# Optimization experiments

Hardware: AMD Instinct MI355X
Metric: run time of the kernel (lower is better)

The kernel has to match this reference:

```python
import math
import jax, jax.numpy as jnp
import numpy as np

N_HEADS = 16
D_EMBED = 1024
D_HEAD = D_EMBED // N_HEADS


def setup_inputs() -> dict:
    key = jax.random.key(0)
    k1, k2, k3, k4, k5 = jax.random.split(key, 5)
    B, S, D = 4, 2048, D_EMBED
    scale = 1.0 / math.sqrt(D)
    return {
        "x": jax.random.normal(k1, (B, S, D), dtype=jnp.float32),
        "in_proj_w": jax.random.normal(k2, (3 * D, D), dtype=jnp.float32) * scale,
        "in_proj_b": jax.random.normal(k3, (3 * D,), dtype=jnp.float32) * 0.02,
        "out_proj_w": jax.random.normal(k4, (D, D), dtype=jnp.float32) * scale,
        "out_proj_b": jax.random.normal(k5, (D,), dtype=jnp.float32) * 0.02,
        "causal_mask": 0,
    }


def reference(x, in_proj_w, in_proj_b, out_proj_w, out_proj_b, causal_mask):
    B, S, D = x.shape
    # in_proj: torch Linear -> x @ W^T + b, then chunk into q,k,v
    qkv = x @ in_proj_w.T + in_proj_b              # [B,S,3D]
    q, k, v = jnp.split(qkv, 3, axis=-1)
    # [B,S,D] -> [B,H,S,d]
    def heads(t):
        return t.reshape(B, S, N_HEADS, D_HEAD).transpose(0, 2, 1, 3)
    q, k, v = heads(q), heads(k), heads(v)
    weight = jnp.einsum("bhsd,bhtd->bhst", q, k)   # [B,H,S,S] materialized scores
    if causal_mask:
        mask = jnp.triu(jnp.ones((S, S), dtype=bool), k=1)
        weight = jnp.where(mask, -jnp.inf, weight)
    weight = jax.nn.softmax(weight / math.sqrt(D_HEAD), axis=-1)
    out = jnp.einsum("bhst,bhtd->bhsd", weight, v)  # [B,H,S,d]
    out = out.transpose(0, 2, 1, 3).reshape(B, S, D)
    return out @ out_proj_w.T + out_proj_b
```

## Files before the change

### kernel.cpp

```cpp
#include <hip/hip_runtime.h>

typedef unsigned short u16;
typedef _Float16 h8 __attribute__((ext_vector_type(8)));
typedef __fp16 fp16x2 __attribute__((ext_vector_type(2)));
typedef float f32x4 __attribute__((ext_vector_type(4)));

constexpr int B_ = 4, S_ = 2048, D_ = 1024, H_ = 16;

__device__ __forceinline__ void async16(const void* g, void* l) {
  __builtin_amdgcn_global_load_lds(
      (const __attribute__((address_space(1))) void*)g,
      (__attribute__((address_space(3))) void*)l, 16, 0, 0);
}

__device__ __forceinline__ unsigned pk2(float a, float b) {
  union { fp16x2 h; unsigned u; } c;
  c.h = __builtin_amdgcn_cvt_pkrtz(a, b);
  return c.u;
}

__global__ __launch_bounds__(256) void cvt_kernel(
    const float* __restrict__ src, _Float16* __restrict__ dst, int n)
{
  const int i = (blockIdx.x * 256 + threadIdx.x) * 4;
  if (i >= n) return;
  const float4 v = *(const float4*)(src + i);
  uint2 o;
  o.x = pk2(v.x, v.y);
  o.y = pk2(v.z, v.w);
  *(uint2*)(dst + i) = o;
}

template<bool OUT_HALF>
__global__ __launch_bounds__(256) void gemm_f16(
    const _Float16* __restrict__ A, const _Float16* __restrict__ Bw,
    const float* __restrict__ bias, void* __restrict__ Cout,
    int M, int N, int K)
{
  __shared__ __align__(16) _Float16 sA[4096];
  __shared__ __align__(16) _Float16 sB[4096];

  const int tid = threadIdx.x;
  const int lane = tid & 63, w = tid >> 6;
  const int wm = w & 1, wn = w >> 1;
  const int m0 = blockIdx.y * 128, n0 = blockIdx.x * 128;

  const int sr = 16 * w + (lane & 15);
  const int ss = lane >> 4;
  const _Float16* gA1 = A + (size_t)(m0 + sr) * K + 8 * ss;
  const _Float16* gA2 = gA1 + (size_t)64 * K;
  const _Float16* gB1 = Bw + (size_t)(n0 + sr) * K + 8 * ss;
  const _Float16* gB2 = gB1 + (size_t)64 * K;
  _Float16* lA1 = &sA[w * 512];
  _Float16* lA2 = &sA[(w + 4) * 512];
  _Float16* lB1 = &sB[w * 512];
  _Float16* lB2 = &sB[(w + 4) * 512];

  const f32x4 zf = {0.f, 0.f, 0.f, 0.f};
  f32x4 acc[4][4];
#pragma unroll
  for (int i = 0; i < 4; ++i)
#pragma unroll
    for (int j = 0; j < 4; ++j) acc[i][j] = zf;

  for (int k0 = 0; k0 < K; k0 += 32) {
    __syncthreads();
    async16(gA1 + k0, lA1);
    async16(gA2 + k0, lA2);
    async16(gB1 + k0, lB1);
    async16(gB2 + k0, lB2);
    __syncthreads();

    h8 fa[4], fb[4];
#pragma unroll
    for (int i = 0; i < 4; ++i) {
      fa[i] = *(const h8*)&sA[((wm * 4 + i) << 9) + (lane << 3)];
      fb[i] = *(const h8*)&sB[((wn * 4 + i) << 9) + (lane << 3)];
    }
#pragma unroll
    for (int i = 0; i < 4; ++i)
#pragma unroll
      for (int j = 0; j < 4; ++j)
        acc[i][j] = __builtin_amdgcn_mfma_f32_16x16x32_f16(fa[i], fb[j], acc[i][j], 0, 0, 0);
  }

  const int g = lane >> 4, cc = lane & 15;
#pragma unroll
  for (int j = 0; j < 4; ++j) {
    const int col = n0 + (wn * 4 + j) * 16 + cc;
    const float bv = bias[col];
#pragma unroll
    for (int i = 0; i < 4; ++i) {
      const int rowb = m0 + (wm * 4 + i) * 16 + g * 4;
#pragma unroll
      for (int r = 0; r < 4; ++r) {
        const float v = acc[i][j][r] + bv;
        if constexpr (OUT_HALF)
          ((_Float16*)Cout)[(size_t)(rowb + r) * N + col] = (_Float16)v;
        else
          ((float*)Cout)[(size_t)(rowb + r) * N + col] = v;
      }
    }
  }
}

__global__ __launch_bounds__(256) void transpose_v(
    const u16* __restrict__ qkv, u16* __restrict__ vT)
{
  __shared__ u16 T[64 * 73];
  const int tid = threadIdx.x;
  const int bh = blockIdx.y, s0 = blockIdx.x * 64;
  const int b = bh >> 4, h = bh & 15;
#pragma unroll
  for (int t = 0; t < 2; ++t) {
    const int c = tid + t * 256, r = c >> 3, cs = c & 7;
    union { int4 v; u16 s[8]; } u;
    u.v = *(const int4*)(qkv + (size_t)(b * S_ + s0 + r) * 3072 + 2048 + h * 64 + 8 * cs);
#pragma unroll
    for (int i = 0; i < 8; ++i) T[r * 73 + 8 * cs + i] = u.s[i];
  }
  __syncthreads();
#pragma unroll
  for (int t = 0; t < 2; ++t) {
    const int c = tid + t * 256, rd = c >> 3, ss = c & 7;
    union { int4 v; u16 s[8]; } u;
#pragma unroll
    for (int i = 0; i < 8; ++i) u.s[i] = T[(8 * ss + i) * 73 + rd];
    *(int4*)(vT + (size_t)(bh * 64 + rd) * S_ + s0 + 8 * ss) = u.v;
  }
}

__global__ __launch_bounds__(256, 4) void attn_f16(
    const _Float16* __restrict__ qkv, const _Float16* __restrict__ vT,
    _Float16* __restrict__ attnO, const int* __restrict__ causal_ptr)
{
  __shared__ __align__(16) _Float16 sQP[9216];
  __shared__ __align__(16) _Float16 sK[4096];
  __shared__ __align__(16) _Float16 sV[4096];

  const int tid = threadIdx.x, lane = tid & 63, w = tid >> 6;
  const int q4 = lane >> 4, cc = lane & 15;
  const int bh = blockIdx.y, b = bh >> 4, h = bh & 15;
  const int q0 = blockIdx.x * 128;
  const int causal = causal_ptr[0];

  {
    const int rr = lane & 15, sc8 = lane >> 4;
#pragma unroll
    for (int tt = 0; tt < 2; ++tt) {
      const int t = 2 * w + tt;
#pragma unroll
      for (int sh = 0; sh < 2; ++sh) {
        const _Float16* g = qkv + (size_t)(b * S_ + q0 + 16 * t + rr) * 3072 + h * 64 + 8 * (4 * sh + sc8);
        async16(g, &sQP[t * 1024 + sh * 512]);
      }
    }
  }
  __syncthreads();

  h8 qf[2][2];
#pragma unroll
  for (int m = 0; m < 2; ++m)
#pragma unroll
    for (int kk = 0; kk < 2; ++kk) {
      h8 v = *(const h8*)&sQP[((2 * w + m) << 10) + (kk << 9) + (lane << 3)];
      qf[m][kk] = v * (_Float16)0.125f;
    }

  h8 ones;
#pragma unroll
  for (int i = 0; i < 8; ++i) ones[i] = (_Float16)1.0f;

  const _Float16* gK = qkv + (size_t)(b * S_ + 16 * w + (lane & 15)) * 3072 + 1024 + h * 64 + 8 * (lane >> 4);
  const _Float16* gV = vT + (size_t)(bh * 64 + 16 * w + (lane & 15)) * S_ + 8 * (lane >> 4);
  _Float16* lK0 = &sK[w * 1024];
  _Float16* lV0 = &sV[w * 1024];

  const int wp = w * 2304;

  const f32x4 zf = {0.f, 0.f, 0.f, 0.f};
  f32x4 oa[2][4], lac[2];
#pragma unroll
  for (int m = 0; m < 2; ++m) {
    lac[m] = zf;
#pragma unroll
    for (int nt = 0; nt < 4; ++nt) oa[m][nt] = zf;
  }

  for (int j0 = 0; j0 < S_; j0 += 64) {
    if (causal && j0 > q0 + 127) break;
    __syncthreads();
    async16(gK + (size_t)j0 * 3072, lK0);
    async16(gK + (size_t)j0 * 3072 + 32, lK0 + 512);
    async16(gV + j0, lV0);
    async16(gV + j0 + 32, lV0 + 512);
    __syncthreads();

    f32x4 sc[2][4];
#pragma unroll
    for (int nt = 0; nt < 4; ++nt) {
      const h8 kf0 = *(const h8*)&sK[(nt << 10) + (lane << 3)];
      const h8 kf1 = *(const h8*)&sK[(nt << 10) + 512 + (lane << 3)];
#pragma unroll
      for (int m = 0; m < 2; ++m) {
        sc[m][nt] = __builtin_amdgcn_mfma_f32_16x16x32_f16(kf0, qf[m][0], zf, 0, 0, 0);
        sc[m][nt] = __builtin_amdgcn_mfma_f32_16x16x32_f16(kf1, qf[m][1], sc[m][nt], 0, 0, 0);
      }
    }

    if (causal) {
#pragma unroll
      for (int m = 0; m < 2; ++m)
#pragma unroll
        for (int nt = 0; nt < 4; ++nt)
#pragma unroll
          for (int r = 0; r < 4; ++r)
            if ((j0 + nt * 16 + q4 * 4 + r) > (q0 + 32 * w + m * 16 + cc))
              sc[m][nt][r] = -1.0e30f;
    }

#pragma unroll
    for (int m = 0; m < 2; ++m)
#pragma unroll
      for (int nt = 0; nt < 4; ++nt) {
        uint2 pk;
        pk.x = pk2(__expf(sc[m][nt][0]), __expf(sc[m][nt][1]));
        pk.y = pk2(__expf(sc[m][nt][2]), __expf(sc[m][nt][3]));
        *(uint2*)&sQP[wp + (m * 16 + cc) * 72 + nt * 16 + q4 * 4] = pk;
      }

    asm volatile("s_waitcnt lgkmcnt(0)" ::: "memory");

    h8 pf[2][2];
#pragma unroll
    for (int m = 0; m < 2; ++m)
#pragma unroll
      for (int kk = 0; kk < 2; ++kk)
        pf[m][kk] = *(const h8*)&sQP[wp + (m * 16 + cc) * 72 + kk * 32 + q4 * 8];

#pragma unroll
    for (int m = 0; m < 2; ++m) {
      lac[m] = __builtin_amdgcn_mfma_f32_16x16x32_f16(pf[m][0], ones, lac[m], 0, 0, 0);
      lac[m] = __builtin_amdgcn_mfma_f32_16x16x32_f16(pf[m][1], ones, lac[m], 0, 0, 0);
    }
#pragma unroll
    for (int nt = 0; nt < 4; ++nt) {
      const h8 vf0 = *(const h8*)&sV[(nt << 10) + (lane << 3)];
      const h8 vf1 = *(const h8*)&sV[(nt << 10) + 512 + (lane << 3)];
#pragma unroll
      for (int m = 0; m < 2; ++m) {
        oa[m][nt] = __builtin_amdgcn_mfma_f32_16x16x32_f16(pf[m][0], vf0, oa[m][nt], 0, 0, 0);
        oa[m][nt] = __builtin_amdgcn_mfma_f32_16x16x32_f16(pf[m][1], vf1, oa[m][nt], 0, 0, 0);
      }
    }
  }

#pragma unroll
  for (int m = 0; m < 2; ++m) {
    float inv[4];
#pragma unroll
    for (int r = 0; r < 4; ++r) inv[r] = 1.0f / lac[m][r];
#pragma unroll
    for (int nt = 0; nt < 4; ++nt) {
      const int col = h * 64 + nt * 16 + cc;
#pragma unroll
      for (int r = 0; r < 4; ++r) {
        const int row = b * S_ + q0 + 32 * w + m * 16 + q4 * 4 + r;
        attnO[(size_t)row * D_ + col] = (_Float16)(oa[m][nt][r] * inv[r]);
      }
    }
  }
}

extern "C" void kernel_launch(void* const* d_in, const int* in_sizes, int n_in,
                              void* d_out, int out_size, void* d_ws, size_t ws_size,
                              hipStream_t stream)
{
  const float* x  = (const float*)d_in[0];
  const float* wi = (const float*)d_in[1];
  const float* bi = (const float*)d_in[2];
  const float* wo = (const float*)d_in[3];
  const float* bo = (const float*)d_in[4];
  const int* causal = (const int*)d_in[5];

  _Float16* xh   = (_Float16*)d_ws;
  _Float16* wih  = xh + 8388608;
  _Float16* woh  = wih + 3145728;
  _Float16* qkvb = woh + 1048576;
  _Float16* vT   = qkvb + 25165824;
  _Float16* attn = vT + 8388608;

  const int M = B_ * S_;

  cvt_kernel<<<8192, 256, 0, stream>>>(x, xh, M * D_);
  cvt_kernel<<<3072, 256, 0, stream>>>(wi, wih, 3 * D_ * D_);
  cvt_kernel<<<1024, 256, 0, stream>>>(wo, woh, D_ * D_);

  gemm_f16<true><<<dim3(24, 64), 256, 0, stream>>>(
      xh, wih, bi, qkvb, M, 3 * D_, D_);

  transpose_v<<<dim3(32, 64), 256, 0, stream>>>((const u16*)qkvb, (u16*)vT);

  attn_f16<<<dim3(16, 64), 256, 0, stream>>>(qkvb, vT, attn, causal);

  gemm_f16<false><<<dim3(8, 64), 256, 0, stream>>>(
      attn, woh, bo, d_out, M, D_, D_);
}
```

Before: 336.0 us.

## Multi-buffer LDS tiles in GEMM and attention to overlap global loads with MFMA

The GEMM switches to a three-stage LDS ring, prefetching two K-tiles ahead with vmcnt-based waits and a single barrier per iteration. The attention kernel double-buffers its K/V tiles, prefetching the next tile while the current one is computed. Both raise wave priority around the MFMA blocks. The aim is to hide global-load latency that the earlier load-sync-compute loops exposed, at the cost of more LDS per block, which may reduce occupancy.

```diff
diff --git a/kernel.cpp b/kernel.cpp
--- a/kernel.cpp
+++ b/kernel.cpp
@@ -37,8 +37,8 @@
     const float* __restrict__ bias, void* __restrict__ Cout,
     int M, int N, int K)
 {
-  __shared__ __align__(16) _Float16 sA[4096];
-  __shared__ __align__(16) _Float16 sB[4096];
+  __shared__ __align__(16) _Float16 sA[3][4096];
+  __shared__ __align__(16) _Float16 sB[3][4096];
 
   const int tid = threadIdx.x;
   const int lane = tid & 63, w = tid >> 6;
@@ -51,10 +51,16 @@
   const _Float16* gA2 = gA1 + (size_t)64 * K;
   const _Float16* gB1 = Bw + (size_t)(n0 + sr) * K + 8 * ss;
   const _Float16* gB2 = gB1 + (size_t)64 * K;
-  _Float16* lA1 = &sA[w * 512];
-  _Float16* lA2 = &sA[(w + 4) * 512];
-  _Float16* lB1 = &sB[w * 512];
-  _Float16* lB2 = &sB[(w + 4) * 512];
+
+  const int nt = K >> 5;
+
+  auto stage = [&](int t, int bb) {
+    const int k0 = t << 5;
+    async16(gA1 + k0, &sA[bb][w * 512]);
+    async16(gA2 + k0, &sA[bb][(w + 4) * 512]);
+    async16(gB1 + k0, &sB[bb][w * 512]);
+    async16(gB2 + k0, &sB[bb][(w + 4) * 512]);
+  };
 
   const f32x4 zf = {0.f, 0.f, 0.f, 0.f};
   f32x4 acc[4][4];
@@ -63,25 +69,38 @@
 #pragma unroll
     for (int j = 0; j < 4; ++j) acc[i][j] = zf;
 
-  for (int k0 = 0; k0 < K; k0 += 32) {
-    __syncthreads();
-    async16(gA1 + k0, lA1);
-    async16(gA2 + k0, lA2);
-    async16(gB1 + k0, lB1);
-    async16(gB2 + k0, lB2);
-    __syncthreads();
-
+  stage(0, 0);
+  stage(1, 1);
+
+  int bt = 0;
+  int bs = 2;
+  for (int t = 0; t < nt; ++t) {
+    if (t < nt - 1) asm volatile("s_waitcnt vmcnt(4)" ::: "memory");
+    else            asm volatile("s_waitcnt vmcnt(0)" ::: "memory");
+    __builtin_amdgcn_s_barrier();
+    asm volatile("" ::: "memory");
+
+    if (t + 2 < nt) stage(t + 2, bs);
+
+    const _Float16* pA = sA[bt];
+    const _Float16* pB = sB[bt];
     h8 fa[4], fb[4];
 #pragma unroll
     for (int i = 0; i < 4; ++i) {
-      fa[i] = *(const h8*)&sA[((wm * 4 + i) << 9) + (lane << 3)];
-      fb[i] = *(const h8*)&sB[((wn * 4 + i) << 9) + (lane << 3)];
-    }
+      fa[i] = *(const h8*)&pA[((wm * 4 + i) << 9) + (lane << 3)];
+      fb[i] = *(const h8*)&pB[((wn * 4 + i) << 9) + (lane << 3)];
+    }
+    __builtin_amdgcn_s_setprio(1);
 #pragma unroll
     for (int i = 0; i < 4; ++i)
 #pragma unroll
       for (int j = 0; j < 4; ++j)
         acc[i][j] = __builtin_amdgcn_mfma_f32_16x16x32_f16(fa[i], fb[j], acc[i][j], 0, 0, 0);
+    __builtin_amdgcn_s_setprio(0);
+    asm volatile("s_waitcnt lgkmcnt(0)" ::: "memory");
+
+    bt = (bt == 2) ? 0 : bt + 1;
+    bs = (bs == 2) ? 0 : bs + 1;
   }
 
   const int g = lane >> 4, cc = lane & 15;
@@ -135,8 +154,8 @@
     _Float16* __restrict__ attnO, const int* __restrict__ causal_ptr)
 {
   __shared__ __align__(16) _Float16 sQP[9216];
-  __shared__ __align__(16) _Float16 sK[4096];
-  __shared__ __align__(16) _Float16 sV[4096];
+  __shared__ __align__(16) _Float16 sK[2][4096];
+  __shared__ __align__(16) _Float16 sV[2][4096];
 
   const int tid = threadIdx.x, lane = tid & 63, w = tid >> 6;
   const int q4 = lane >> 4, cc = lane & 15;
@@ -144,6 +163,9 @@
   const int q0 = blockIdx.x * 128;
   const int causal = causal_ptr[0];
 
+  const _Float16* gK = qkv + (size_t)(b * S_ + 16 * w + (lane & 15)) * 3072 + 1024 + h * 64 + 8 * (lane >> 4);
+  const _Float16* gV = vT + (size_t)(bh * 64 + 16 * w + (lane & 15)) * S_ + 8 * (lane >> 4);
+
   {
     const int rr = lane & 15, sc8 = lane >> 4;
 #pragma unroll
@@ -156,6 +178,11 @@
       }
     }
   }
+  async16(gK, &sK[0][w * 1024]);
+  async16(gK + 32, &sK[0][w * 1024 + 512]);
+  async16(gV, &sV[0][w * 1024]);
+  async16(gV + 32, &sV[0][w * 1024 + 512]);
+
   __syncthreads();
 
   h8 qf[2][2];
@@ -166,15 +193,11 @@
       h8 v = *(const h8*)&sQP[((2 * w + m) << 10) + (kk << 9) + (lane << 3)];
       qf[m][kk] = v * (_Float16)0.125f;
     }
+  asm volatile("s_waitcnt lgkmcnt(0)" ::: "memory");
 
   h8 ones;
 #pragma unroll
   for (int i = 0; i < 8; ++i) ones[i] = (_Float16)1.0f;
-
-  const _Float16* gK = qkv + (size_t)(b * S_ + 16 * w + (lane & 15)) * 3072 + 1024 + h * 64 + 8 * (lane >> 4);
-  const _Float16* gV = vT + (size_t)(bh * 64 + 16 * w + (lane & 15)) * S_ + 8 * (lane >> 4);
-  _Float16* lK0 = &sK[w * 1024];
-  _Float16* lV0 = &sV[w * 1024];
 
   const int wp = w * 2304;
 
@@ -187,20 +210,34 @@
     for (int nt = 0; nt < 4; ++nt) oa[m][nt] = zf;
   }
 
-  for (int j0 = 0; j0 < S_; j0 += 64) {
-    if (causal && j0 > q0 + 127) break;
-    __syncthreads();
-    async16(gK + (size_t)j0 * 3072, lK0);
-    async16(gK + (size_t)j0 * 3072 + 32, lK0 + 512);
-    async16(gV + j0, lV0);
-    async16(gV + j0 + 32, lV0 + 512);
-    __syncthreads();
+  const int jend = causal ? (q0 + 128) : S_;
+  const int ktiles = jend >> 6;
+
+  for (int t = 0; t < ktiles; ++t) {
+    const int j0 = t << 6;
+    const int bb = t & 1;
+
+    if (t + 1 < ktiles) {
+      const size_t j1 = (size_t)(j0 + 64);
+      async16(gK + j1 * 3072, &sK[bb ^ 1][w * 1024]);
+      async16(gK + j1 * 3072 + 32, &sK[bb ^ 1][w * 1024 + 512]);
+      async16(gV + j1, &sV[bb ^ 1][w * 1024]);
+      async16(gV + j1 + 32, &sV[bb ^ 1][w * 1024 + 512]);
+      asm volatile("s_waitcnt vmcnt(4)" ::: "memory");
+    } else {
+      asm volatile("s_waitcnt vmcnt(0)" ::: "memory");
+    }
+    __builtin_amdgcn_s_barrier();
+    asm volatile("" ::: "memory");
+
+    const _Float16* pK = sK[bb];
+    const _Float16* pV = sV[bb];
 
     f32x4 sc[2][4];
 #pragma unroll
     for (int nt = 0; nt < 4; ++nt) {
-      const h8 kf0 = *(const h8*)&sK[(nt << 10) + (lane << 3)];
-      const h8 kf1 = *(const h8*)&sK[(nt << 10) + 512 + (lane << 3)];
+      const h8 kf0 = *(const h8*)&pK[(nt << 10) + (lane << 3)];
+      const h8 kf1 = *(const h8*)&pK[(nt << 10) + 512 + (lane << 3)];
 #pragma unroll
       for (int m = 0; m < 2; ++m) {
         sc[m][nt] = __builtin_amdgcn_mfma_f32_16x16x32_f16(kf0, qf[m][0], zf, 0, 0, 0);
@@ -238,6 +275,7 @@
       for (int kk = 0; kk < 2; ++kk)
         pf[m][kk] = *(const h8*)&sQP[wp + (m * 16 + cc) * 72 + kk * 32 + q4 * 8];
 
+    __builtin_amdgcn_s_setprio(1);
 #pragma unroll
     for (int m = 0; m < 2; ++m) {
       lac[m] = __builtin_amdgcn_mfma_f32_16x16x32_f16(pf[m][0], ones, lac[m], 0, 0, 0);
@@ -245,14 +283,18 @@
     }
 #pragma unroll
     for (int nt = 0; nt < 4; ++nt) {
-      const h8 vf0 = *(const h8*)&sV[(nt << 10) + (lane << 3)];
-      const h8 vf1 = *(const h8*)&sV[(nt << 10) + 512 + (lane << 3)];
+      const h8 vf0 = *(const h8*)&pV[(nt << 10) + (lane << 3)];
+      const h8 vf1 = *(const h8*)&pV[(nt << 10) + 512 + (lane << 3)];
 #pragma unroll
       for (int m = 0; m < 2; ++m) {
         oa[m][nt] = __builtin_amdgcn_mfma_f32_16x16x32_f16(pf[m][0], vf0, oa[m][nt], 0, 0, 0);
         oa[m][nt] = __builtin_amdgcn_mfma_f32_16x16x32_f16(pf[m][1], vf1, oa[m][nt], 0, 0, 0);
       }
     }
+    __builtin_amdgcn_s_setprio(0);
+
+    asm volatile("s_waitcnt lgkmcnt(0)" ::: "memory");
+    __builtin_amdgcn_s_barrier();
   }
 
 #pragma unroll
```

Result: slower. 361.6 us (+7.6%).

## Register-prefetch K/V tiles in attention loop and merge conversion kernels

Applied to the files above, without the earlier changes.

The attention loop now loads the next K/V tile from global memory into registers while the current tile is being computed, then stores those registers into LDS. This replaces the direct async global-to-LDS copies that were bracketed by two barriers. MFMA sections are wrapped in s_setprio to raise wave priority, and the three fp32-to-fp16 conversion launches are merged into a single kernel to save launch overhead. The prefetch costs extra VGPRs, which could lower occupancy.

```diff
diff --git a/kernel.cpp b/kernel.cpp
--- a/kernel.cpp
+++ b/kernel.cpp
@@ -19,11 +19,19 @@
   return c.u;
 }
 
-__global__ __launch_bounds__(256) void cvt_kernel(
-    const float* __restrict__ src, _Float16* __restrict__ dst, int n)
-{
-  const int i = (blockIdx.x * 256 + threadIdx.x) * 4;
-  if (i >= n) return;
+__global__ __launch_bounds__(256) void cvt3_kernel(
+    const float* __restrict__ x, const float* __restrict__ wi,
+    const float* __restrict__ wo, _Float16* __restrict__ xh,
+    _Float16* __restrict__ wih, _Float16* __restrict__ woh)
+{
+  const int bid = blockIdx.x;
+  const float* src;
+  _Float16* dst;
+  int base;
+  if (bid < 8192)       { src = x;  dst = xh;  base = bid; }
+  else if (bid < 11264) { src = wi; dst = wih; base = bid - 8192; }
+  else                  { src = wo; dst = woh; base = bid - 11264; }
+  const int i = (base * 256 + threadIdx.x) * 4;
   const float4 v = *(const float4*)(src + i);
   uint2 o;
   o.x = pk2(v.x, v.y);
@@ -156,6 +164,15 @@
       }
     }
   }
+
+  const _Float16* gK = qkv + (size_t)(b * S_ + 16 * w + (lane & 15)) * 3072 + 1024 + h * 64 + 8 * (lane >> 4);
+  const _Float16* gV = vT + (size_t)(bh * 64 + 16 * w + (lane & 15)) * S_ + 8 * (lane >> 4);
+
+  int4 rK0 = *(const int4*)gK;
+  int4 rK1 = *(const int4*)(gK + 32);
+  int4 rV0 = *(const int4*)gV;
+  int4 rV1 = *(const int4*)(gV + 32);
+
   __syncthreads();
 
   h8 qf[2][2];
@@ -171,11 +188,6 @@
 #pragma unroll
   for (int i = 0; i < 8; ++i) ones[i] = (_Float16)1.0f;
 
-  const _Float16* gK = qkv + (size_t)(b * S_ + 16 * w + (lane & 15)) * 3072 + 1024 + h * 64 + 8 * (lane >> 4);
-  const _Float16* gV = vT + (size_t)(bh * 64 + 16 * w + (lane & 15)) * S_ + 8 * (lane >> 4);
-  _Float16* lK0 = &sK[w * 1024];
-  _Float16* lV0 = &sV[w * 1024];
-
   const int wp = w * 2304;
 
   const f32x4 zf = {0.f, 0.f, 0.f, 0.f};
@@ -187,16 +199,33 @@
     for (int nt = 0; nt < 4; ++nt) oa[m][nt] = zf;
   }
 
-  for (int j0 = 0; j0 < S_; j0 += 64) {
-    if (causal && j0 > q0 + 127) break;
-    __syncthreads();
-    async16(gK + (size_t)j0 * 3072, lK0);
-    async16(gK + (size_t)j0 * 3072 + 32, lK0 + 512);
-    async16(gV + j0, lV0);
-    async16(gV + j0 + 32, lV0 + 512);
-    __syncthreads();
+  const int jend = causal ? (q0 + 128) : S_;
+  const int ktiles = jend >> 6;
+
+  for (int t = 0; t < ktiles; ++t) {
+    const int j0 = t << 6;
+
+    asm volatile("s_waitcnt lgkmcnt(0)" ::: "memory");
+    __builtin_amdgcn_s_barrier();
+
+    *(int4*)&sK[w * 1024 + lane * 8] = rK0;
+    *(int4*)&sK[w * 1024 + 512 + lane * 8] = rK1;
+    *(int4*)&sV[w * 1024 + lane * 8] = rV0;
+    *(int4*)&sV[w * 1024 + 512 + lane * 8] = rV1;
+
+    if (t + 1 < ktiles) {
+      const size_t j1 = (size_t)(j0 + 64);
+      rK0 = *(const int4*)(gK + j1 * 3072);
+      rK1 = *(const int4*)(gK + j1 * 3072 + 32);
+      rV0 = *(const int4*)(gV + j1);
+      rV1 = *(const int4*)(gV + j1 + 32);
+    }
+
+    asm volatile("s_waitcnt lgkmcnt(0)" ::: "memory");
+    __builtin_amdgcn_s_barrier();
 
     f32x4 sc[2][4];
+    __builtin_amdgcn_s_setprio(1);
 #pragma unroll
     for (int nt = 0; nt < 4; ++nt) {
       const h8 kf0 = *(const h8*)&sK[(nt << 10) + (lane << 3)];
@@ -207,6 +236,7 @@
         sc[m][nt] = __builtin_amdgcn_mfma_f32_16x16x32_f16(kf1, qf[m][1], sc[m][nt], 0, 0, 0);
       }
     }
+    __builtin_amdgcn_s_setprio(0);
 
     if (causal) {
 #pragma unroll
@@ -238,6 +268,7 @@
       for (int kk = 0; kk < 2; ++kk)
         pf[m][kk] = *(const h8*)&sQP[wp + (m * 16 + cc) * 72 + kk * 32 + q4 * 8];
 
+    __builtin_amdgcn_s_setprio(1);
 #pragma unroll
     for (int m = 0; m < 2; ++m) {
       lac[m] = __builtin_amdgcn_mfma_f32_16x16x32_f16(pf[m][0], ones, lac[m], 0, 0, 0);
@@ -253,6 +284,7 @@
         oa[m][nt] = __builtin_amdgcn_mfma_f32_16x16x32_f16(pf[m][1], vf1, oa[m][nt], 0, 0, 0);
       }
     }
+    __builtin_amdgcn_s_setprio(0);
   }
 
 #pragma unroll
@@ -292,9 +324,7 @@
 
   const int M = B_ * S_;
 
-  cvt_kernel<<<8192, 256, 0, stream>>>(x, xh, M * D_);
-  cvt_kernel<<<3072, 256, 0, stream>>>(wi, wih, 3 * D_ * D_);
-  cvt_kernel<<<1024, 256, 0, stream>>>(wo, woh, D_ * D_);
+  cvt3_kernel<<<12288, 256, 0, stream>>>(x, wi, wo, xh, wih, woh);
 
   gemm_f16<true><<<dim3(24, 64), 256, 0, stream>>>(
       xh, wih, bi, qkvb, M, 3 * D_, D_);
```

After: 398.4 us. +18.6%, slower.

## Use 256x256 double-buffered GEMM tiles with swizzled block order, fuse converts

Applied to the files above, without the earlier changes.

Replaces the 128x128 single-buffered fp16 GEMM with a 512-thread, 256x256-tile kernel. It uses a K step of 64 and double-buffered LDS filled by async global-to-LDS loads, which are interleaved with the MFMA phases under setprio and barriers. Block IDs are swizzled so neighbouring blocks share inputs in cache. The three fp32-to-fp16 conversion launches are merged into one kernel. The large 128KB LDS footprint allows only one block per CU, and the grids shrink to 384 and 128 blocks, which risks tail imbalance and leaves CUs idle on the output projection.

```diff
diff --git a/kernel.cpp b/kernel.cpp
--- a/kernel.cpp
+++ b/kernel.cpp
@@ -19,11 +19,19 @@
   return c.u;
 }
 
-__global__ __launch_bounds__(256) void cvt_kernel(
-    const float* __restrict__ src, _Float16* __restrict__ dst, int n)
-{
-  const int i = (blockIdx.x * 256 + threadIdx.x) * 4;
-  if (i >= n) return;
+__global__ __launch_bounds__(256) void cvt3_kernel(
+    const float* __restrict__ x, const float* __restrict__ wi,
+    const float* __restrict__ wo, _Float16* __restrict__ xh,
+    _Float16* __restrict__ wih, _Float16* __restrict__ woh)
+{
+  const int bid = blockIdx.x;
+  const float* src;
+  _Float16* dst;
+  int base;
+  if (bid < 8192)       { src = x;  dst = xh;  base = bid; }
+  else if (bid < 11264) { src = wi; dst = wih; base = bid - 8192; }
+  else                  { src = wo; dst = woh; base = bid - 11264; }
+  const int i = (base * 256 + threadIdx.x) * 4;
   const float4 v = *(const float4*)(src + i);
   uint2 o;
   o.x = pk2(v.x, v.y);
@@ -32,69 +40,115 @@
 }
 
 template<bool OUT_HALF>
-__global__ __launch_bounds__(256) void gemm_f16(
+__global__ __launch_bounds__(512, 2) void gemm256_f16(
     const _Float16* __restrict__ A, const _Float16* __restrict__ Bw,
     const float* __restrict__ bias, void* __restrict__ Cout,
     int M, int N, int K)
 {
-  __shared__ __align__(16) _Float16 sA[4096];
-  __shared__ __align__(16) _Float16 sB[4096];
+  __shared__ __align__(16) _Float16 sA[2][16384];
+  __shared__ __align__(16) _Float16 sB[2][16384];
 
   const int tid = threadIdx.x;
   const int lane = tid & 63, w = tid >> 6;
-  const int wm = w & 1, wn = w >> 1;
-  const int m0 = blockIdx.y * 128, n0 = blockIdx.x * 128;
-
-  const int sr = 16 * w + (lane & 15);
-  const int ss = lane >> 4;
-  const _Float16* gA1 = A + (size_t)(m0 + sr) * K + 8 * ss;
-  const _Float16* gA2 = gA1 + (size_t)64 * K;
-  const _Float16* gB1 = Bw + (size_t)(n0 + sr) * K + 8 * ss;
-  const _Float16* gB2 = gB1 + (size_t)64 * K;
-  _Float16* lA1 = &sA[w * 512];
-  _Float16* lA2 = &sA[(w + 4) * 512];
-  _Float16* lB1 = &sB[w * 512];
-  _Float16* lB2 = &sB[(w + 4) * 512];
+  const int wm = w >> 2, wn = w & 3;
+
+  const int id = blockIdx.x;
+  const int cpx = gridDim.x >> 3;
+  const int swz = (id & 7) * cpx + (id >> 3);
+  const int nbx = N >> 8;
+  const int bx = swz % nbx, by = swz / nbx;
+  const int m0 = by * 256, n0 = bx * 256;
+
+  const int r15 = lane & 15, s4 = lane >> 4;
+  const _Float16* gA[4];
+  const _Float16* gB[4];
+  int lofs[4];
+#pragma unroll
+  for (int j = 0; j < 4; ++j) {
+    const int t = 2 * w + (j >> 1), kk = j & 1;
+    gA[j] = A + (size_t)(m0 + 16 * t + r15) * K + kk * 32 + s4 * 8;
+    gB[j] = Bw + (size_t)(n0 + 16 * t + r15) * K + kk * 32 + s4 * 8;
+    lofs[j] = (t * 2 + kk) * 512;
+  }
 
   const f32x4 zf = {0.f, 0.f, 0.f, 0.f};
-  f32x4 acc[4][4];
-#pragma unroll
-  for (int i = 0; i < 4; ++i)
+  f32x4 acc[8][4];
+#pragma unroll
+  for (int i = 0; i < 8; ++i)
 #pragma unroll
     for (int j = 0; j < 4; ++j) acc[i][j] = zf;
 
-  for (int k0 = 0; k0 < K; k0 += 32) {
-    __syncthreads();
-    async16(gA1 + k0, lA1);
-    async16(gA2 + k0, lA2);
-    async16(gB1 + k0, lB1);
-    async16(gB2 + k0, lB2);
-    __syncthreads();
-
-    h8 fa[4], fb[4];
-#pragma unroll
-    for (int i = 0; i < 4; ++i) {
-      fa[i] = *(const h8*)&sA[((wm * 4 + i) << 9) + (lane << 3)];
-      fb[i] = *(const h8*)&sB[((wn * 4 + i) << 9) + (lane << 3)];
-    }
-#pragma unroll
-    for (int i = 0; i < 4; ++i)
-#pragma unroll
-      for (int j = 0; j < 4; ++j)
-        acc[i][j] = __builtin_amdgcn_mfma_f32_16x16x32_f16(fa[i], fb[j], acc[i][j], 0, 0, 0);
+#pragma unroll
+  for (int j = 0; j < 4; ++j) { async16(gA[j], &sA[0][lofs[j]]); async16(gB[j], &sB[0][lofs[j]]); }
+#pragma unroll
+  for (int j = 0; j < 4; ++j) { async16(gA[j] + 64, &sA[1][lofs[j]]); async16(gB[j] + 64, &sB[1][lofs[j]]); }
+  asm volatile("s_waitcnt vmcnt(8)" ::: "memory");
+  __builtin_amdgcn_s_barrier();
+
+  const int NT = K >> 6;
+  for (int kt = 0; kt < NT; ++kt) {
+    const int cb = kt & 1;
+    const _Float16* pA = sA[cb];
+    const _Float16* pB = sB[cb];
+    const bool pre = (kt >= 1) && (kt + 1 < NT);
+    const int ko = (kt + 1) * 64;
+    _Float16* nA = sA[cb ^ 1];
+    _Float16* nB = sB[cb ^ 1];
+
+    h8 fb[4][2];
+#pragma unroll
+    for (int p = 0; p < 4; ++p) {
+      h8 fa[2][2];
+      if (p == 0) {
+#pragma unroll
+        for (int nt = 0; nt < 4; ++nt)
+#pragma unroll
+          for (int kk = 0; kk < 2; ++kk)
+            fb[nt][kk] = *(const h8*)&pB[((wn * 4 + nt) * 2 + kk) * 512 + lane * 8];
+      }
+#pragma unroll
+      for (int i = 0; i < 2; ++i)
+#pragma unroll
+        for (int kk = 0; kk < 2; ++kk)
+          fa[i][kk] = *(const h8*)&pA[((wm * 8 + 2 * p + i) * 2 + kk) * 512 + lane * 8];
+
+      if (pre) {
+        if (p == 0) { async16(gA[0] + ko, &nA[lofs[0]]); async16(gA[1] + ko, &nA[lofs[1]]); async16(gB[0] + ko, &nB[lofs[0]]); }
+        if (p == 1) { async16(gA[2] + ko, &nA[lofs[2]]); async16(gA[3] + ko, &nA[lofs[3]]); async16(gB[1] + ko, &nB[lofs[1]]); }
+        if (p == 2) { async16(gB[2] + ko, &nB[lofs[2]]); async16(gB[3] + ko, &nB[lofs[3]]); }
+      }
+
+      __builtin_amdgcn_s_barrier();
+      __builtin_amdgcn_s_setprio(1);
+#pragma unroll
+      for (int i = 0; i < 2; ++i)
+#pragma unroll
+        for (int nt = 0; nt < 4; ++nt)
+#pragma unroll
+          for (int kk = 0; kk < 2; ++kk)
+            acc[2 * p + i][nt] = __builtin_amdgcn_mfma_f32_16x16x32_f16(
+                fa[i][kk], fb[nt][kk], acc[2 * p + i][nt], 0, 0, 0);
+      __builtin_amdgcn_s_setprio(0);
+      if (p < 3) __builtin_amdgcn_s_barrier();
+    }
+
+    if (kt + 1 < NT) {
+      asm volatile("s_waitcnt vmcnt(0)" ::: "memory");
+      __builtin_amdgcn_s_barrier();
+    }
   }
 
   const int g = lane >> 4, cc = lane & 15;
 #pragma unroll
-  for (int j = 0; j < 4; ++j) {
-    const int col = n0 + (wn * 4 + j) * 16 + cc;
+  for (int nt = 0; nt < 4; ++nt) {
+    const int col = n0 + wn * 64 + nt * 16 + cc;
     const float bv = bias[col];
 #pragma unroll
-    for (int i = 0; i < 4; ++i) {
-      const int rowb = m0 + (wm * 4 + i) * 16 + g * 4;
+    for (int mt = 0; mt < 8; ++mt) {
+      const int rowb = m0 + wm * 128 + mt * 16 + g * 4;
 #pragma unroll
       for (int r = 0; r < 4; ++r) {
-        const float v = acc[i][j][r] + bv;
+        const float v = acc[mt][nt][r] + bv;
         if constexpr (OUT_HALF)
           ((_Float16*)Cout)[(size_t)(rowb + r) * N + col] = (_Float16)v;
         else
@@ -292,17 +346,15 @@
 
   const int M = B_ * S_;
 
-  cvt_kernel<<<8192, 256, 0, stream>>>(x, xh, M * D_);
-  cvt_kernel<<<3072, 256, 0, stream>>>(wi, wih, 3 * D_ * D_);
-  cvt_kernel<<<1024, 256, 0, stream>>>(wo, woh, D_ * D_);
-
-  gemm_f16<true><<<dim3(24, 64), 256, 0, stream>>>(
+  cvt3_kernel<<<12288, 256, 0, stream>>>(x, wi, wo, xh, wih, woh);
+
+  gemm256_f16<true><<<384, 512, 0, stream>>>(
       xh, wih, bi, qkvb, M, 3 * D_, D_);
 
   transpose_v<<<dim3(32, 64), 256, 0, stream>>>((const u16*)qkvb, (u16*)vT);
 
   attn_f16<<<dim3(16, 64), 256, 0, stream>>>(qkvb, vT, attn, causal);
 
-  gemm_f16<false><<<dim3(8, 64), 256, 0, stream>>>(
+  gemm256_f16<false><<<128, 512, 0, stream>>>(
       attn, woh, bo, d_out, M, D_, D_);
 }
```

Measured after the change: 324.8 us. 3.3% less time.
